# Kernel tuning notes

Measured on AMD Instinct MI355X. Metric: run time of the kernel, lower is better.

Reference implementation:

```python
import jax, jax.numpy as jnp
import numpy as np
from jax import lax

DILATIONS = [1, 2, 4, 8, 16, 32, 64, 128, 256, 512]
L = len(DILATIONS)
T = 2048          # input_size (== sequence length)
C = 128           # residual channels
COND = 16         # condition vector dim
B = 8


def conv1d(x, w, dilation=1):
    # x: [B, T, Cin], w: [K, Cin, Cout] (WIO), SAME padding like keras Conv1D
    return lax.conv_general_dilated(
        x, w, window_strides=(1,), padding='SAME',
        rhs_dilation=(dilation,), dimension_numbers=('NWC', 'WIO', 'NWC'))


def setup_inputs() -> dict:
    key = jax.random.key(0)
    ks = iter(jax.random.split(key, 32))
    n = lambda shape, s=0.05: jax.random.normal(next(ks), shape, dtype=jnp.float32) * s
    inp = {
        'x': jax.random.normal(next(ks), (B, T, 1), dtype=jnp.float32),
        'condition': jax.random.normal(next(ks), (B, COND), dtype=jnp.float32),
        # input projection Conv1D(128, 1)
        'Wc': n((1, 1, C)), 'bc': jnp.zeros((C,), jnp.float32),
        # per-block dilated gated convs Conv1D(128, 3), stacked over L blocks
        'Wt': n((L, 3, C, C)), 'bt': jnp.zeros((L, C), jnp.float32),
        'Ws': n((L, 3, C, C)), 'bs': jnp.zeros((L, C), jnp.float32),
        # stacked conditioning Dense weights: 128 Dense(cond->T) per branch per block
        # Dense i weight [COND, T]; stacked & transposed -> [L, COND, T, 128]
        'Dt': n((L, COND, T, C)), 'Bt': jnp.zeros((L, T, C), jnp.float32),
        'Ds': n((L, COND, T, C)), 'Bs': jnp.zeros((L, T, C), jnp.float32),
        # skip / residual 1x1 convs
        'Wskip': n((L, 1, C, C)), 'bskip': jnp.zeros((L, C), jnp.float32),
        'Wres': n((L, 1, C, C)), 'bres': jnp.zeros((L, C), jnp.float32),
        # output head
        'W1': n((3, C, 2048)), 'b1': jnp.zeros((2048,), jnp.float32),
        'W2': n((3, 2048, 256)), 'b2': jnp.zeros((256,), jnp.float32),
        'W3': n((1, 256, 1)), 'b3': jnp.zeros((1,), jnp.float32),
    }
    return inp


def reference(x, condition, Wc, bc, Wt, bt, Ws, bs, Dt, Bt, Ds, Bs,
              Wskip, bskip, Wres, bres, W1, b1, W2, b2, W3, b3):
    h = conv1d(x, Wc) + bc  # [B, T, 128]
    skip_sum = jnp.zeros_like(h)
    for l, d in enumerate(DILATIONS):
        # fused equivalent of 128 per-channel Dense layers + concat:
        # trans[b,t,k] = condition[b,:] @ Dense_k.W + Dense_k.b
        tt = jnp.einsum('bc,ctk->btk', condition, Dt[l]) + Bt[l]
        ts = jnp.einsum('bc,ctk->btk', condition, Ds[l]) + Bs[l]
        g = jnp.tanh(conv1d(h, Wt[l], d) + bt[l] + tt) * \
            jax.nn.sigmoid(conv1d(h, Ws[l], d) + bs[l] + ts)
        skip_sum = skip_sum + conv1d(g, Wskip[l]) + bskip[l]
        h = conv1d(g, Wres[l]) + bres[l] + h
    out = jax.nn.relu(conv1d(skip_sum, W1) + b1)  # [B, T, 2048]
    out = jax.nn.relu(conv1d(out, W2) + b2)       # [B, T, 256]
    out = jnp.tanh(conv1d(out, W3) + b3)          # [B, T, 1]
    return out
```

## Files before the change

kernel.cpp:

```cpp
#include <hip/hip_runtime.h>
#include <hip/hip_bf16.h>
#include <math.h>

#define T 2048
#define C 128
#define BATCH 8
#define NLAYER 10

typedef short bf16x8 __attribute__((ext_vector_type(8)));
typedef float f32x4 __attribute__((ext_vector_type(4)));
typedef unsigned short u16x4 __attribute__((ext_vector_type(4)));

__device__ __forceinline__ float sigmoidf_(float x) {
    return 1.f / (1.f + __expf(-x));
}
__device__ __forceinline__ float tanhf_(float x) {
    float a = fabsf(x);
    float e = __expf(-2.f * a);
    float t = (1.f - e) / (1.f + e);
    return copysignf(t, x);
}
__device__ __forceinline__ ushort f2bf(float v) {
    __hip_bfloat16 h = __float2bfloat16(v);
    return *reinterpret_cast<ushort*>(&h);
}
__device__ __forceinline__ float bf2f(ushort u) {
    unsigned int x = ((unsigned int)u) << 16;
    return __uint_as_float(x);
}
__device__ __forceinline__ void gl_lds16(const ushort* g, ushort* l) {
    __builtin_amdgcn_global_load_lds(
        (const __attribute__((address_space(1))) unsigned int*)g,
        (__attribute__((address_space(3))) unsigned int*)l, 16, 0, 0);
}

__global__ void k_init(const float* __restrict__ x, const float* __restrict__ Wc,
                       const float* __restrict__ bc, float* __restrict__ h32,
                       ushort* __restrict__ hb, float* __restrict__ skip) {
    int i = blockIdx.x * 256 + threadIdx.x;
    int c = i & 127;
    int pos = i >> 7;
    float v = x[pos] * Wc[c] + bc[c];
    h32[i] = v;
    hb[i] = f2bf(v);
    skip[i] = 0.f;
}

__global__ void k_prep_wgT(const float* __restrict__ Wt, const float* __restrict__ Ws,
                           ushort* __restrict__ WGb) {
    const int tx = threadIdx.x, ty = threadIdx.y;
    const int z = blockIdx.z, s = z & 1, lj = z >> 1;
    const int l = lj / 3, j = lj % 3;
    const float* src = (s ? Ws : Wt) + (size_t)lj * 128 * 128;
    const int col0 = blockIdx.x * 32, ci0 = blockIdx.y * 32;
    __shared__ float tile[32][33];
    #pragma unroll
    for (int i = 0; i < 4; ++i)
        tile[ty + i * 8][tx] = src[(size_t)(ci0 + ty + i * 8) * 128 + col0 + tx];
    __syncthreads();
    #pragma unroll
    for (int i = 0; i < 4; ++i)
        WGb[((size_t)l * 256 + s * 128 + col0 + ty + i * 8) * 384 + j * 128 + ci0 + tx] =
            f2bf(tile[tx][ty + i * 8]);
}
__global__ void k_prep_wrT(const float* __restrict__ Wskip, const float* __restrict__ Wres,
                           ushort* __restrict__ WRb) {
    const int tx = threadIdx.x, ty = threadIdx.y;
    const int z = blockIdx.z, s = z & 1, l = z >> 1;
    const float* src = (s ? Wres : Wskip) + (size_t)l * 128 * 128;
    const int col0 = blockIdx.x * 32, ci0 = blockIdx.y * 32;
    __shared__ float tile[32][33];
    #pragma unroll
    for (int i = 0; i < 4; ++i)
        tile[ty + i * 8][tx] = src[(size_t)(ci0 + ty + i * 8) * 128 + col0 + tx];
    __syncthreads();
    #pragma unroll
    for (int i = 0; i < 4; ++i)
        WRb[((size_t)l * 256 + s * 128 + col0 + ty + i * 8) * 128 + ci0 + tx] =
            f2bf(tile[tx][ty + i * 8]);
}
template<int R>
__global__ void k_prep_wT(const float* __restrict__ W, ushort* __restrict__ Wb, int N) {
    const int tx = threadIdx.x, ty = threadIdx.y;
    const int x = blockIdx.x * 32 + tx;
    const int y0 = blockIdx.y * 32;
    __shared__ float tile[32][33];
    #pragma unroll
    for (int i = 0; i < 4; ++i)
        tile[ty + i * 8][tx] = W[(size_t)(y0 + ty + i * 8) * N + x];
    __syncthreads();
    const int n0 = blockIdx.x * 32;
    #pragma unroll
    for (int i = 0; i < 4; ++i)
        Wb[(size_t)(n0 + ty + i * 8) * R + y0 + tx] = f2bf(tile[tx][ty + i * 8]);
}

__global__ void k_skip_pad(const float* __restrict__ in, ushort* __restrict__ skipp) {
    int i = blockIdx.x * 256 + threadIdx.x;
    int b = i >> 18, rem = i & 262143;
    skipp[(size_t)b * 262400 + 128 + rem] = f2bf(in[i]);
}
__global__ void k_zero_pads(ushort* __restrict__ out1p, ushort* __restrict__ skipp) {
    int i = blockIdx.x * 256 + threadIdx.x;
    if (i < 16384) {
        int ri = i >> 10, col = i & 1023;
        int b = ri >> 1, pr = (ri & 1) ? 2049 : 0;
        ((unsigned int*)out1p)[((size_t)b * 2050 + pr) * 1024 + col] = 0u;
    } else {
        int j = i - 16384;
        int ri = j >> 6, col = j & 63;
        int b = ri >> 1, pr = (ri & 1) ? 2049 : 0;
        ((unsigned int*)skipp)[((size_t)b * 2050 + pr) * 64 + col] = 0u;
    }
}

__global__ __launch_bounds__(256) void k_cond(
    const float* __restrict__ cond,
    const float* __restrict__ Dt, const float* __restrict__ Bt,
    const float* __restrict__ Ds, const float* __restrict__ Bs,
    const float* __restrict__ bt, const float* __restrict__ bs,
    ushort* __restrict__ z0, int l0)
{
    const int br = blockIdx.z;
    const float* D  = br ? Ds : Dt;
    const float* B_ = br ? Bs : Bt;
    const float* b_ = br ? bs : bt;
    const int l  = l0 + blockIdx.y;
    const int ll = blockIdx.y;
    const int k4 = (threadIdx.x & 31) * 4;
    const int tq = threadIdx.x >> 5;
    const int t  = blockIdx.x * 8 + tq;

    __shared__ float sc[128];
    if (threadIdx.x < 128) sc[threadIdx.x] = cond[threadIdx.x];
    __syncthreads();

    const f32x4 bv = *(const f32x4*)(b_ + l * 128 + k4);
    const f32x4 Bv = *(const f32x4*)(B_ + ((size_t)l * T + t) * 128 + k4);

    f32x4 z[8];
    #pragma unroll
    for (int b = 0; b < 8; ++b) z[b] = bv + Bv;

    const float* dp = D + (((size_t)l * 16) * T + t) * 128 + k4;
    #pragma unroll
    for (int c = 0; c < 16; ++c) {
        const f32x4 dv = *(const f32x4*)(dp + (size_t)c * T * 128);
        #pragma unroll
        for (int b = 0; b < 8; ++b)
            z[b] += sc[b * 16 + c] * dv;
    }

    #pragma unroll
    for (int b = 0; b < 8; ++b) {
        size_t zb = (((size_t)ll * 8 + b) * T + t) * 256;
        u16x4 p;
        #pragma unroll
        for (int j = 0; j < 4; ++j) p[j] = f2bf(z[b][j]);
        *(u16x4*)(z0 + zb + br * 128 + k4) = p;
    }
}

__global__ __launch_bounds__(256) void k_gate(
    const float* __restrict__ h32_in, float* __restrict__ h32_out,
    const ushort* __restrict__ hb_in, ushort* __restrict__ hb_out,
    float* __restrict__ skip32,
    const ushort* __restrict__ WG,
    const ushort* __restrict__ WR,
    const ushort* __restrict__ z0l,
    const float* __restrict__ bskip, const float* __restrict__ bres,
    int d)
{
    __shared__ ushort lds[3 * 32 * 136];
    const int tid  = threadIdx.x;
    const int lane = tid & 63, ln16 = lane & 15, quad = lane >> 4;
    const int wave = tid >> 6;
    const int n_off = wave * 64;
    const int t0 = blockIdx.x * 4;

    #pragma unroll
    for (int it = 0; it < 6; ++it) {
        int task = tid + it * 256;
        int part = task & 15;
        int r = (task >> 4) & 31;
        int j = task >> 9;
        int t = t0 + (r >> 3) + (j - 1) * d;
        int b = r & 7;
        uint4 v = make_uint4(0u, 0u, 0u, 0u);
        if (t >= 0 && t < T) v = *(const uint4*)(hb_in + ((size_t)b * T + t) * 128 + part * 8);
        *(uint4*)(&lds[(j * 32 + r) * 136 + part * 8]) = v;
    }
    __syncthreads();

    f32x4 acc[2][4];
    #pragma unroll
    for (int mt = 0; mt < 2; ++mt)
        #pragma unroll
        for (int nt = 0; nt < 4; ++nt)
            acc[mt][nt] = (f32x4){0.f, 0.f, 0.f, 0.f};

    #pragma unroll
    for (int j = 0; j < 3; ++j) {
        #pragma unroll
        for (int kc = 0; kc < 4; ++kc) {
            bf16x8 af[2], bfr[4];
            #pragma unroll
            for (int mt = 0; mt < 2; ++mt)
                af[mt] = *(const bf16x8*)(&lds[(j * 32 + mt * 16 + ln16) * 136 + kc * 32 + quad * 8]);
            #pragma unroll
            for (int nt = 0; nt < 4; ++nt)
                bfr[nt] = *(const bf16x8*)(WG + (size_t)(n_off + nt * 16 + ln16) * 384 + j * 128 + kc * 32 + quad * 8);
            #pragma unroll
            for (int mt = 0; mt < 2; ++mt)
                #pragma unroll
                for (int nt = 0; nt < 4; ++nt)
                    acc[mt][nt] = __builtin_amdgcn_mfma_f32_16x16x32_bf16(af[mt], bfr[nt], acc[mt][nt], 0, 0, 0);
        }
    }
    __syncthreads();

    #pragma unroll
    for (int mt = 0; mt < 2; ++mt) {
        #pragma unroll
        for (int nt = 0; nt < 4; ++nt) {
            int n = n_off + nt * 16 + ln16;
            #pragma unroll
            for (int r4 = 0; r4 < 4; ++r4) {
                int row = mt * 16 + quad * 4 + r4;
                int b = row & 7, p = row >> 3;
                float z = acc[mt][nt][r4] + bf2f(z0l[((size_t)b * T + t0 + p) * 256 + n]);
                lds[row * 264 + n] = f2bf(z);
            }
        }
    }
    __syncthreads();

    {
        int r = tid >> 3;
        int k0 = (tid & 7) * 16;
        #pragma unroll
        for (int kk = 0; kk < 16; ++kk) {
            int k = k0 + kk;
            float zt = bf2f(lds[r * 264 + k]);
            float zs = bf2f(lds[r * 264 + 128 + k]);
            lds[8704 + r * 136 + k] = f2bf(tanhf_(zt) * sigmoidf_(zs));
        }
    }
    __syncthreads();

    f32x4 acc2[2][4];
    #pragma unroll
    for (int mt = 0; mt < 2; ++mt)
        #pragma unroll
        for (int nt = 0; nt < 4; ++nt)
            acc2[mt][nt] = (f32x4){0.f, 0.f, 0.f, 0.f};

    #pragma unroll
    for (int kc = 0; kc < 4; ++kc) {
        bf16x8 af[2], bfr[4];
        #pragma unroll
        for (int mt = 0; mt < 2; ++mt)
            af[mt] = *(const bf16x8*)(&lds[8704 + (mt * 16 + ln16) * 136 + kc * 32 + quad * 8]);
        #pragma unroll
        for (int nt = 0; nt < 4; ++nt)
            bfr[nt] = *(const bf16x8*)(WR + (size_t)(n_off + nt * 16 + ln16) * 128 + kc * 32 + quad * 8);
        #pragma unroll
        for (int mt = 0; mt < 2; ++mt)
            #pragma unroll
            for (int nt = 0; nt < 4; ++nt)
                acc2[mt][nt] = __builtin_amdgcn_mfma_f32_16x16x32_bf16(af[mt], bfr[nt], acc2[mt][nt], 0, 0, 0);
    }

    #pragma unroll
    for (int mt = 0; mt < 2; ++mt) {
        #pragma unroll
        for (int nt = 0; nt < 4; ++nt) {
            int n = n_off + nt * 16 + ln16;
            int k = n & 127;
            #pragma unroll
            for (int r4 = 0; r4 < 4; ++r4) {
                int row = mt * 16 + quad * 4 + r4;
                int b = row & 7, p = row >> 3;
                size_t idx = ((size_t)b * T + t0 + p) * 128 + k;
                float v = acc2[mt][nt][r4];
                if (n < 128) {
                    skip32[idx] += v + bskip[k];
                } else {
                    float hv = v + bres[k] + h32_in[idx];
                    h32_out[idx] = hv;
                    hb_out[idx] = f2bf(hv);
                }
            }
        }
    }
}

#define CV2_AUS 8704
#define CV2_BUF 33280

__global__ __launch_bounds__(256) void k_conv1t(
    const ushort* __restrict__ A,
    const ushort* __restrict__ Wb,
    const float* __restrict__ bias,
    ushort* __restrict__ out1p)
{
    __shared__ ushort sh[2 * CV2_BUF];
    const int tid  = threadIdx.x;
    const int lane = tid & 63, ln16 = lane & 15, quad = lane >> 4;
    const int wave = tid >> 6;
    const int wm = wave >> 1, wn = wave & 1;
    const int m0 = blockIdx.x * 128;
    const int b  = blockIdx.y;
    const int n0 = blockIdx.z * 128;
    const size_t aRow0 = (size_t)b * 2050 + m0;

    f32x4 acc[4][4];
    #pragma unroll
    for (int i = 0; i < 4; ++i)
        #pragma unroll
        for (int j = 0; j < 4; ++j) acc[i][j] = (f32x4){0.f, 0.f, 0.f, 0.f};

    auto stage = [&](int d, int c) {
        const int sb = d * CV2_BUF;
        const int k0 = c * 64;
        #pragma unroll
        for (int ps = 0; ps < 4; ++ps) {
            int task = ps * 256 + tid;
            int r = task >> 3, p = task & 7, q = p ^ (r & 7);
            gl_lds16(A + (aRow0 + r) * 128 + k0 + q * 8,
                     &sh[sb + ((ps * 256 + wave * 64) << 3)]);
        }
        if (tid < 64) {
            int task = 1024 + tid;
            int r = task >> 3, p = task & 7, q = p ^ (r & 7);
            gl_lds16(A + (aRow0 + r) * 128 + k0 + q * 8,
                     &sh[sb + (1024 << 3)]);
        }
        #pragma unroll
        for (int ps = 0; ps < 12; ++ps) {
            int task = ps * 256 + tid;
            int rb = task >> 3, p = task & 7, q = p ^ (rb & 7);
            int nl = rb & 127, tap = rb >> 7;
            gl_lds16(Wb + (size_t)(n0 + nl) * 384 + tap * 128 + k0 + q * 8,
                     &sh[sb + CV2_AUS + ((ps * 256 + wave * 64) << 3)]);
        }
    };

    stage(0, 0);
    __syncthreads();

    for (int c = 0; c < 2; ++c) {
        if (c == 0) stage(1, 1);
        const int sb = (c & 1) * CV2_BUF;
        #pragma unroll
        for (int j = 0; j < 3; ++j) {
            #pragma unroll
            for (int kk = 0; kk < 2; ++kk) {
                bf16x8 af[4], bfr[4];
                #pragma unroll
                for (int mt = 0; mt < 4; ++mt) {
                    int r = wm * 64 + mt * 16 + ln16 + j;
                    int s = (kk << 2) | quad;
                    af[mt] = *(const bf16x8*)(&sh[sb + r * 64 + ((s ^ (r & 7)) << 3)]);
                }
                #pragma unroll
                for (int nt = 0; nt < 4; ++nt) {
                    int rb = j * 128 + wn * 64 + nt * 16 + ln16;
                    int s = (kk << 2) | quad;
                    bfr[nt] = *(const bf16x8*)(&sh[sb + CV2_AUS + rb * 64 + ((s ^ (rb & 7)) << 3)]);
                }
                #pragma unroll
                for (int mt = 0; mt < 4; ++mt)
                    #pragma unroll
                    for (int nt = 0; nt < 4; ++nt)
                        acc[mt][nt] = __builtin_amdgcn_mfma_f32_16x16x32_bf16(af[mt], bfr[nt], acc[mt][nt], 0, 0, 0);
            }
        }
        __syncthreads();
    }

    #pragma unroll
    for (int nt = 0; nt < 4; ++nt) {
        int n = n0 + wn * 64 + nt * 16 + ln16;
        float bv = bias[n];
        #pragma unroll
        for (int mt = 0; mt < 4; ++mt) {
            #pragma unroll
            for (int r4 = 0; r4 < 4; ++r4) {
                int m = wm * 64 + mt * 16 + quad * 4 + r4;
                int t = m0 + m;
                float v = fmaxf(acc[mt][nt][r4] + bv, 0.f);
                out1p[((size_t)b * 2050 + 1 + t) * 2048 + n] = f2bf(v);
            }
        }
    }
}

__global__ __launch_bounds__(256) void k_conv2t(
    const ushort* __restrict__ A,
    const ushort* __restrict__ Wb,
    const float* __restrict__ bias,
    float* __restrict__ out2)
{
    __shared__ ushort sh[2 * CV2_BUF];
    const int tid  = threadIdx.x;
    const int lane = tid & 63, ln16 = lane & 15, quad = lane >> 4;
    const int wave = tid >> 6;
    const int wm = wave >> 1, wn = wave & 1;
    const int m0 = blockIdx.x * 128;
    const int b  = blockIdx.y;
    const int n0 = blockIdx.z * 128;
    const size_t aRow0 = (size_t)b * 2050 + m0;

    f32x4 acc[4][4];
    #pragma unroll
    for (int i = 0; i < 4; ++i)
        #pragma unroll
        for (int j = 0; j < 4; ++j) acc[i][j] = (f32x4){0.f, 0.f, 0.f, 0.f};

    auto stage = [&](int d, int cc) {
        const int sb = d * CV2_BUF;
        const int k0 = cc * 64;
        #pragma unroll
        for (int ps = 0; ps < 4; ++ps) {
            int task = ps * 256 + tid;
            int r = task >> 3, p = task & 7, q = p ^ (r & 7);
            gl_lds16(A + (aRow0 + r) * 2048 + k0 + q * 8,
                     &sh[sb + ((ps * 256 + wave * 64) << 3)]);
        }
        if (tid < 64) {
            int task = 1024 + tid;
            int r = task >> 3, p = task & 7, q = p ^ (r & 7);
            gl_lds16(A + (aRow0 + r) * 2048 + k0 + q * 8,
                     &sh[sb + (1024 << 3)]);
        }
        #pragma unroll
        for (int ps = 0; ps < 12; ++ps) {
            int task = ps * 256 + tid;
            int rb = task >> 3, p = task & 7, q = p ^ (rb & 7);
            int nl = rb & 127, tap = rb >> 7;
            gl_lds16(Wb + (size_t)(n0 + nl) * 6144 + tap * 2048 + k0 + q * 8,
                     &sh[sb + CV2_AUS + ((ps * 256 + wave * 64) << 3)]);
        }
    };

    stage(0, 0);
    __syncthreads();

    for (int cc = 0; cc < 32; ++cc) {
        if (cc < 31) stage((cc + 1) & 1, cc + 1);
        const int sb = (cc & 1) * CV2_BUF;
        #pragma unroll
        for (int j = 0; j < 3; ++j) {
            #pragma unroll
            for (int kk = 0; kk < 2; ++kk) {
                bf16x8 af[4], bfr[4];
                #pragma unroll
                for (int mt = 0; mt < 4; ++mt) {
                    int r = wm * 64 + mt * 16 + ln16 + j;
                    int s = (kk << 2) | quad;
                    af[mt] = *(const bf16x8*)(&sh[sb + r * 64 + ((s ^ (r & 7)) << 3)]);
                }
                #pragma unroll
                for (int nt = 0; nt < 4; ++nt) {
                    int rb = j * 128 + wn * 64 + nt * 16 + ln16;
                    int s = (kk << 2) | quad;
                    bfr[nt] = *(const bf16x8*)(&sh[sb + CV2_AUS + rb * 64 + ((s ^ (rb & 7)) << 3)]);
                }
                #pragma unroll
                for (int mt = 0; mt < 4; ++mt)
                    #pragma unroll
                    for (int nt = 0; nt < 4; ++nt)
                        acc[mt][nt] = __builtin_amdgcn_mfma_f32_16x16x32_bf16(af[mt], bfr[nt], acc[mt][nt], 0, 0, 0);
            }
        }
        __syncthreads();
    }

    #pragma unroll
    for (int nt = 0; nt < 4; ++nt) {
        int n = n0 + wn * 64 + nt * 16 + ln16;
        float bv = bias[n];
        #pragma unroll
        for (int mt = 0; mt < 4; ++mt) {
            #pragma unroll
            for (int r4 = 0; r4 < 4; ++r4) {
                int m = wm * 64 + mt * 16 + quad * 4 + r4;
                int t = m0 + m;
                float v = fmaxf(acc[mt][nt][r4] + bv, 0.f);
                out2[((size_t)b * T + t) * 256 + n] = v;
            }
        }
    }
}

__global__ __launch_bounds__(256) void k_conv3(
    const float* __restrict__ out2, const float* __restrict__ W3,
    const float* __restrict__ b3, float* __restrict__ out)
{
    int wid = threadIdx.x >> 6, lane = threadIdx.x & 63;
    int pos = blockIdx.x * 4 + wid;
    float4 v = *(const float4*)(out2 + (size_t)pos * 256 + lane * 4);
    float4 w = *(const float4*)(W3 + lane * 4);
    float sum = v.x * w.x + v.y * w.y + v.z * w.z + v.w * w.w;
    #pragma unroll
    for (int off = 32; off > 0; off >>= 1) sum += __shfl_down(sum, off);
    if (lane == 0) out[pos] = tanhf_(sum + b3[0]);
}

extern "C" void kernel_launch(void* const* d_in, const int* in_sizes, int n_in,
                              void* d_out, int out_size, void* d_ws, size_t ws_size,
                              hipStream_t stream)
{
    const float* x     = (const float*)d_in[0];
    const float* cond  = (const float*)d_in[1];
    const float* Wc    = (const float*)d_in[2];
    const float* bc    = (const float*)d_in[3];
    const float* Wt    = (const float*)d_in[4];
    const float* bt    = (const float*)d_in[5];
    const float* Ws    = (const float*)d_in[6];
    const float* bs    = (const float*)d_in[7];
    const float* Dt    = (const float*)d_in[8];
    const float* Bt    = (const float*)d_in[9];
    const float* Ds    = (const float*)d_in[10];
    const float* Bs    = (const float*)d_in[11];
    const float* Wskip = (const float*)d_in[12];
    const float* bskip = (const float*)d_in[13];
    const float* Wres  = (const float*)d_in[14];
    const float* bres  = (const float*)d_in[15];
    const float* W1    = (const float*)d_in[16];
    const float* b1    = (const float*)d_in[17];
    const float* W2    = (const float*)d_in[18];
    const float* b2    = (const float*)d_in[19];
    const float* W3    = (const float*)d_in[20];
    const float* b3    = (const float*)d_in[21];
    float* out = (float*)d_out;

    float* ws = (float*)d_ws;
    float*  skip32 = ws;
    float*  h32a   = ws + 2097152;
    float*  h32b   = ws + 4194304;
    float*  out2   = ws + 6291456;
    ushort* u      = (ushort*)(ws + 10485760);
    ushort* hba    = u;
    ushort* hbb    = u + 2097152;
    ushort* WGb    = u + 4194304;
    ushort* WRb    = u + 5177344;
    ushort* W1b    = u + 5505024;
    ushort* W2b    = u + 6291456;
    ushort* skipp  = u;
    ushort* z0     = u + 9961472;
    ushort* out1p  = u + 7864320;

    k_init<<<8192, 256, 0, stream>>>(x, Wc, bc, h32a, hba, skip32);
    k_prep_wgT<<<dim3(4, 4, 60), dim3(32, 8), 0, stream>>>(Wt, Ws, WGb);
    k_prep_wrT<<<dim3(4, 4, 20), dim3(32, 8), 0, stream>>>(Wskip, Wres, WRb);
    k_prep_wT<384><<<dim3(64, 12), dim3(32, 8), 0, stream>>>(W1, W1b, 2048);
    k_prep_wT<6144><<<dim3(8, 192), dim3(32, 8), 0, stream>>>(W2, W2b, 256);

    static const int DIL[NLAYER] = {1, 2, 4, 8, 16, 32, 64, 128, 256, 512};
    float*  h32in = h32a;  float*  h32out = h32b;
    ushort* hbin  = hba;   ushort* hbout  = hbb;

    for (int chunk = 0; chunk < 2; ++chunk) {
        int l0 = chunk * 5;
        k_cond<<<dim3(T / 8, 5, 2), 256, 0, stream>>>(cond, Dt, Bt, Ds, Bs, bt, bs, z0, l0);
        for (int l = l0; l < l0 + 5; ++l) {
            k_gate<<<512, 256, 0, stream>>>(
                h32in, h32out, hbin, hbout, skip32,
                WGb + (size_t)l * 256 * 384,
                WRb + (size_t)l * 256 * 128,
                z0 + (size_t)(l - l0) * 8 * T * 256,
                bskip + l * 128, bres + l * 128,
                DIL[l]);
            float* tf = h32in; h32in = h32out; h32out = tf;
            ushort* tu = hbin; hbin = hbout; hbout = tu;
        }
    }

    k_skip_pad<<<8192, 256, 0, stream>>>(skip32, skipp);
    k_zero_pads<<<68, 256, 0, stream>>>(out1p, skipp);
    k_conv1t<<<dim3(16, 8, 16), 256, 0, stream>>>(skipp, W1b, b1, out1p);
    k_conv2t<<<dim3(16, 8, 2), 256, 0, stream>>>(out1p, W2b, b2, out2);
    k_conv3<<<(BATCH * T) / 4, 256, 0, stream>>>(out2, W3, b3, out);
}
```

Baseline: 868.5 us.

## Defer skip projections into one batched K=1280 GEMM after the residual stack

```diff
diff --git a/kernel.cpp b/kernel.cpp
--- a/kernel.cpp
+++ b/kernel.cpp
@@ -10,6 +10,8 @@
 typedef short bf16x8 __attribute__((ext_vector_type(8)));
 typedef float f32x4 __attribute__((ext_vector_type(4)));
 typedef unsigned short u16x4 __attribute__((ext_vector_type(4)));
+
+struct GPtrs { const ushort* p[NLAYER]; };
 
 __device__ __forceinline__ float sigmoidf_(float x) {
     return 1.f / (1.f + __expf(-x));
@@ -36,14 +38,13 @@
 
 __global__ void k_init(const float* __restrict__ x, const float* __restrict__ Wc,
                        const float* __restrict__ bc, float* __restrict__ h32,
-                       ushort* __restrict__ hb, float* __restrict__ skip) {
+                       ushort* __restrict__ hb) {
     int i = blockIdx.x * 256 + threadIdx.x;
     int c = i & 127;
     int pos = i >> 7;
     float v = x[pos] * Wc[c] + bc[c];
     h32[i] = v;
     hb[i] = f2bf(v);
-    skip[i] = 0.f;
 }
 
 __global__ void k_prep_wgT(const float* __restrict__ Wt, const float* __restrict__ Ws,
@@ -59,12 +60,14 @@
         tile[ty + i * 8][tx] = src[(size_t)(ci0 + ty + i * 8) * 128 + col0 + tx];
     __syncthreads();
     #pragma unroll
-    for (int i = 0; i < 4; ++i)
-        WGb[((size_t)l * 256 + s * 128 + col0 + ty + i * 8) * 384 + j * 128 + ci0 + tx] =
-            f2bf(tile[tx][ty + i * 8]);
-}
-__global__ void k_prep_wrT(const float* __restrict__ Wskip, const float* __restrict__ Wres,
-                           ushort* __restrict__ WRb) {
+    for (int i = 0; i < 4; ++i) {
+        int col = col0 + ty + i * 8;
+        int np = ((col >> 4) * 32) + s * 16 + (col & 15);
+        WGb[((size_t)l * 256 + np) * 384 + j * 128 + ci0 + tx] = f2bf(tile[tx][ty + i * 8]);
+    }
+}
+__global__ void k_prep_wr2(const float* __restrict__ Wskip, const float* __restrict__ Wres,
+                           ushort* __restrict__ WSKb, ushort* __restrict__ WRESb) {
     const int tx = threadIdx.x, ty = threadIdx.y;
     const int z = blockIdx.z, s = z & 1, l = z >> 1;
     const float* src = (s ? Wres : Wskip) + (size_t)l * 128 * 128;
@@ -75,9 +78,12 @@
         tile[ty + i * 8][tx] = src[(size_t)(ci0 + ty + i * 8) * 128 + col0 + tx];
     __syncthreads();
     #pragma unroll
-    for (int i = 0; i < 4; ++i)
-        WRb[((size_t)l * 256 + s * 128 + col0 + ty + i * 8) * 128 + ci0 + tx] =
-            f2bf(tile[tx][ty + i * 8]);
+    for (int i = 0; i < 4; ++i) {
+        int n = col0 + ty + i * 8, ci = ci0 + tx;
+        ushort v = f2bf(tile[tx][ty + i * 8]);
+        if (s) WRESb[((size_t)l * 128 + n) * 128 + ci] = v;
+        else   WSKb[(size_t)n * 1280 + l * 128 + ci] = v;
+    }
 }
 template<int R>
 __global__ void k_prep_wT(const float* __restrict__ W, ushort* __restrict__ Wb, int N) {
@@ -95,11 +101,6 @@
         Wb[(size_t)(n0 + ty + i * 8) * R + y0 + tx] = f2bf(tile[tx][ty + i * 8]);
 }
 
-__global__ void k_skip_pad(const float* __restrict__ in, ushort* __restrict__ skipp) {
-    int i = blockIdx.x * 256 + threadIdx.x;
-    int b = i >> 18, rem = i & 262143;
-    skipp[(size_t)b * 262400 + 128 + rem] = f2bf(in[i]);
-}
 __global__ void k_zero_pads(ushort* __restrict__ out1p, ushort* __restrict__ skipp) {
     int i = blockIdx.x * 256 + threadIdx.x;
     if (i < 16384) {
@@ -151,24 +152,25 @@
             z[b] += sc[b * 16 + c] * dv;
     }
 
+    const int np = ((k4 >> 4) * 32) + br * 16 + (k4 & 15);
     #pragma unroll
     for (int b = 0; b < 8; ++b) {
         size_t zb = (((size_t)ll * 8 + b) * T + t) * 256;
         u16x4 p;
         #pragma unroll
         for (int j = 0; j < 4; ++j) p[j] = f2bf(z[b][j]);
-        *(u16x4*)(z0 + zb + br * 128 + k4) = p;
+        *(u16x4*)(z0 + zb + np) = p;
     }
 }
 
 __global__ __launch_bounds__(256) void k_gate(
     const float* __restrict__ h32_in, float* __restrict__ h32_out,
     const ushort* __restrict__ hb_in, ushort* __restrict__ hb_out,
-    float* __restrict__ skip32,
     const ushort* __restrict__ WG,
-    const ushort* __restrict__ WR,
+    const ushort* __restrict__ WRES,
     const ushort* __restrict__ z0l,
-    const float* __restrict__ bskip, const float* __restrict__ bres,
+    ushort* __restrict__ gout,
+    const float* __restrict__ bres,
     int d)
 {
     __shared__ ushort lds[3 * 32 * 136];
@@ -190,6 +192,23 @@
         if (t >= 0 && t < T) v = *(const uint4*)(hb_in + ((size_t)b * T + t) * 128 + part * 8);
         *(uint4*)(&lds[(j * 32 + r) * 136 + part * 8]) = v;
     }
+
+    ushort zre[2][4][4];
+    float hpre[2][2][4];
+    #pragma unroll
+    for (int mt = 0; mt < 2; ++mt) {
+        #pragma unroll
+        for (int r4 = 0; r4 < 4; ++r4) {
+            int row = mt * 16 + quad * 4 + r4;
+            int b = row & 7, p = row >> 3;
+            const ushort* zp = z0l + ((size_t)b * T + t0 + p) * 256 + n_off + ln16;
+            #pragma unroll
+            for (int nt = 0; nt < 4; ++nt) zre[mt][nt][r4] = zp[nt * 16];
+            const float* hp = h32_in + ((size_t)b * T + t0 + p) * 128 + wave * 32 + ln16;
+            #pragma unroll
+            for (int n2 = 0; n2 < 2; ++n2) hpre[mt][n2][r4] = hp[n2 * 16];
+        }
+    }
     __syncthreads();
 
     f32x4 acc[2][4];
@@ -217,79 +236,162 @@
                     acc[mt][nt] = __builtin_amdgcn_mfma_f32_16x16x32_bf16(af[mt], bfr[nt], acc[mt][nt], 0, 0, 0);
         }
     }
-    __syncthreads();
-
-    #pragma unroll
-    for (int mt = 0; mt < 2; ++mt) {
-        #pragma unroll
-        for (int nt = 0; nt < 4; ++nt) {
-            int n = n_off + nt * 16 + ln16;
+
+    ushort gfr[2][2][4];
+    #pragma unroll
+    for (int mt = 0; mt < 2; ++mt)
+        #pragma unroll
+        for (int i = 0; i < 2; ++i)
+            #pragma unroll
+            for (int r4 = 0; r4 < 4; ++r4) {
+                float zt = acc[mt][2 * i][r4]     + bf2f(zre[mt][2 * i][r4]);
+                float zs = acc[mt][2 * i + 1][r4] + bf2f(zre[mt][2 * i + 1][r4]);
+                gfr[mt][i][r4] = f2bf(tanhf_(zt) * sigmoidf_(zs));
+            }
+    #pragma unroll
+    for (int mt = 0; mt < 2; ++mt)
+        #pragma unroll
+        for (int i = 0; i < 2; ++i)
             #pragma unroll
             for (int r4 = 0; r4 < 4; ++r4) {
                 int row = mt * 16 + quad * 4 + r4;
                 int b = row & 7, p = row >> 3;
-                float z = acc[mt][nt][r4] + bf2f(z0l[((size_t)b * T + t0 + p) * 256 + n]);
-                lds[row * 264 + n] = f2bf(z);
-            }
-        }
-    }
-    __syncthreads();
-
-    {
-        int r = tid >> 3;
-        int k0 = (tid & 7) * 16;
-        #pragma unroll
-        for (int kk = 0; kk < 16; ++kk) {
-            int k = k0 + kk;
-            float zt = bf2f(lds[r * 264 + k]);
-            float zs = bf2f(lds[r * 264 + 128 + k]);
-            lds[8704 + r * 136 + k] = f2bf(tanhf_(zt) * sigmoidf_(zs));
-        }
-    }
-    __syncthreads();
-
-    f32x4 acc2[2][4];
+                gout[((size_t)b * T + t0 + p) * 128 + wave * 32 + i * 16 + ln16] = gfr[mt][i][r4];
+            }
+    __syncthreads();
+
     #pragma unroll
     for (int mt = 0; mt < 2; ++mt)
         #pragma unroll
-        for (int nt = 0; nt < 4; ++nt)
-            acc2[mt][nt] = (f32x4){0.f, 0.f, 0.f, 0.f};
+        for (int i = 0; i < 2; ++i)
+            #pragma unroll
+            for (int r4 = 0; r4 < 4; ++r4) {
+                int row = mt * 16 + quad * 4 + r4;
+                lds[8704 + row * 136 + wave * 32 + i * 16 + ln16] = gfr[mt][i][r4];
+            }
+    __syncthreads();
+
+    f32x4 acc2[2][2];
+    #pragma unroll
+    for (int mt = 0; mt < 2; ++mt)
+        #pragma unroll
+        for (int n2 = 0; n2 < 2; ++n2)
+            acc2[mt][n2] = (f32x4){0.f, 0.f, 0.f, 0.f};
 
     #pragma unroll
     for (int kc = 0; kc < 4; ++kc) {
-        bf16x8 af[2], bfr[4];
+        bf16x8 af[2], bfr[2];
         #pragma unroll
         for (int mt = 0; mt < 2; ++mt)
             af[mt] = *(const bf16x8*)(&lds[8704 + (mt * 16 + ln16) * 136 + kc * 32 + quad * 8]);
         #pragma unroll
-        for (int nt = 0; nt < 4; ++nt)
-            bfr[nt] = *(const bf16x8*)(WR + (size_t)(n_off + nt * 16 + ln16) * 128 + kc * 32 + quad * 8);
+        for (int n2 = 0; n2 < 2; ++n2)
+            bfr[n2] = *(const bf16x8*)(WRES + (size_t)(wave * 32 + n2 * 16 + ln16) * 128 + kc * 32 + quad * 8);
         #pragma unroll
         for (int mt = 0; mt < 2; ++mt)
             #pragma unroll
-            for (int nt = 0; nt < 4; ++nt)
-                acc2[mt][nt] = __builtin_amdgcn_mfma_f32_16x16x32_bf16(af[mt], bfr[nt], acc2[mt][nt], 0, 0, 0);
-    }
-
-    #pragma unroll
-    for (int mt = 0; mt < 2; ++mt) {
-        #pragma unroll
-        for (int nt = 0; nt < 4; ++nt) {
-            int n = n_off + nt * 16 + ln16;
-            int k = n & 127;
+            for (int n2 = 0; n2 < 2; ++n2)
+                acc2[mt][n2] = __builtin_amdgcn_mfma_f32_16x16x32_bf16(af[mt], bfr[n2], acc2[mt][n2], 0, 0, 0);
+    }
+
+    #pragma unroll
+    for (int n2 = 0; n2 < 2; ++n2) {
+        int n = wave * 32 + n2 * 16 + ln16;
+        float bv = bres[n];
+        #pragma unroll
+        for (int mt = 0; mt < 2; ++mt) {
             #pragma unroll
             for (int r4 = 0; r4 < 4; ++r4) {
                 int row = mt * 16 + quad * 4 + r4;
                 int b = row & 7, p = row >> 3;
-                size_t idx = ((size_t)b * T + t0 + p) * 128 + k;
-                float v = acc2[mt][nt][r4];
-                if (n < 128) {
-                    skip32[idx] += v + bskip[k];
-                } else {
-                    float hv = v + bres[k] + h32_in[idx];
-                    h32_out[idx] = hv;
-                    hb_out[idx] = f2bf(hv);
-                }
+                size_t idx = ((size_t)b * T + t0 + p) * 128 + n;
+                float hv = acc2[mt][n2][r4] + bv + hpre[mt][n2][r4];
+                h32_out[idx] = hv;
+                hb_out[idx] = f2bf(hv);
+            }
+        }
+    }
+}
+
+__global__ __launch_bounds__(256) void k_skipsum(
+    GPtrs gp, const ushort* __restrict__ Wsk,
+    const float* __restrict__ bskip,
+    ushort* __restrict__ skipp)
+{
+    __shared__ ushort sh[2 * 12288];
+    const int tid  = threadIdx.x;
+    const int lane = tid & 63, ln16 = lane & 15, quad = lane >> 4;
+    const int wave = tid >> 6;
+    const int wm = wave >> 1, wn = wave & 1;
+    const int m0 = blockIdx.x * 64;
+    const int b  = blockIdx.y;
+
+    f32x4 acc[2][4];
+    #pragma unroll
+    for (int i = 0; i < 2; ++i)
+        #pragma unroll
+        for (int j = 0; j < 4; ++j) acc[i][j] = (f32x4){0.f, 0.f, 0.f, 0.f};
+
+    auto stage = [&](int dd, int kc) {
+        const int sb = dd * 12288;
+        const int l = kc >> 1, k0 = (kc & 1) * 64;
+        const ushort* gl = gp.p[l] + ((size_t)b * T + m0) * 128 + k0;
+        #pragma unroll
+        for (int ps = 0; ps < 2; ++ps) {
+            int task = ps * 256 + tid;
+            int r = task >> 3, p = task & 7, q = p ^ (r & 7);
+            gl_lds16(gl + (size_t)r * 128 + q * 8, &sh[sb + ((ps * 256 + wave * 64) << 3)]);
+        }
+        #pragma unroll
+        for (int ps = 0; ps < 4; ++ps) {
+            int task = ps * 256 + tid;
+            int r = task >> 3, p = task & 7, q = p ^ (r & 7);
+            gl_lds16(Wsk + (size_t)r * 1280 + l * 128 + k0 + q * 8,
+                     &sh[sb + 4096 + ((ps * 256 + wave * 64) << 3)]);
+        }
+    };
+
+    stage(0, 0);
+    __syncthreads();
+
+    for (int kc = 0; kc < 20; ++kc) {
+        if (kc < 19) stage((kc + 1) & 1, kc + 1);
+        const int sb = (kc & 1) * 12288;
+        #pragma unroll
+        for (int kk = 0; kk < 2; ++kk) {
+            bf16x8 af[2], bfr[4];
+            int s = (kk << 2) | quad;
+            #pragma unroll
+            for (int mt = 0; mt < 2; ++mt) {
+                int r = wm * 32 + mt * 16 + ln16;
+                af[mt] = *(const bf16x8*)(&sh[sb + r * 64 + ((s ^ (r & 7)) << 3)]);
+            }
+            #pragma unroll
+            for (int nt = 0; nt < 4; ++nt) {
+                int rb = wn * 64 + nt * 16 + ln16;
+                bfr[nt] = *(const bf16x8*)(&sh[sb + 4096 + rb * 64 + ((s ^ (rb & 7)) << 3)]);
+            }
+            #pragma unroll
+            for (int mt = 0; mt < 2; ++mt)
+                #pragma unroll
+                for (int nt = 0; nt < 4; ++nt)
+                    acc[mt][nt] = __builtin_amdgcn_mfma_f32_16x16x32_bf16(af[mt], bfr[nt], acc[mt][nt], 0, 0, 0);
+        }
+        __syncthreads();
+    }
+
+    #pragma unroll
+    for (int nt = 0; nt < 4; ++nt) {
+        int n = wn * 64 + nt * 16 + ln16;
+        float bv = 0.f;
+        #pragma unroll
+        for (int l = 0; l < NLAYER; ++l) bv += bskip[l * 128 + n];
+        #pragma unroll
+        for (int mt = 0; mt < 2; ++mt) {
+            #pragma unroll
+            for (int r4 = 0; r4 < 4; ++r4) {
+                int t = m0 + wm * 32 + mt * 16 + quad * 4 + r4;
+                skipp[((size_t)b * 2050 + 1 + t) * 128 + n] = f2bf(acc[mt][nt][r4] + bv);
             }
         }
     }
@@ -320,8 +422,8 @@
         #pragma unroll
         for (int j = 0; j < 4; ++j) acc[i][j] = (f32x4){0.f, 0.f, 0.f, 0.f};
 
-    auto stage = [&](int d, int c) {
-        const int sb = d * CV2_BUF;
+    auto stage = [&](int dd, int c) {
+        const int sb = dd * CV2_BUF;
         const int k0 = c * 64;
         #pragma unroll
         for (int ps = 0; ps < 4; ++ps) {
@@ -418,8 +520,8 @@
         #pragma unroll
         for (int j = 0; j < 4; ++j) acc[i][j] = (f32x4){0.f, 0.f, 0.f, 0.f};
 
-    auto stage = [&](int d, int cc) {
-        const int sb = d * CV2_BUF;
+    auto stage = [&](int dd, int cc) {
+        const int sb = dd * CV2_BUF;
         const int k0 = cc * 64;
         #pragma unroll
         for (int ps = 0; ps < 4; ++ps) {
@@ -536,25 +638,31 @@
     const float* b3    = (const float*)d_in[21];
     float* out = (float*)d_out;
 
-    float* ws = (float*)d_ws;
-    float*  skip32 = ws;
-    float*  h32a   = ws + 2097152;
-    float*  h32b   = ws + 4194304;
-    float*  out2   = ws + 6291456;
-    ushort* u      = (ushort*)(ws + 10485760);
-    ushort* hba    = u;
-    ushort* hbb    = u + 2097152;
-    ushort* WGb    = u + 4194304;
-    ushort* WRb    = u + 5177344;
-    ushort* W1b    = u + 5505024;
-    ushort* W2b    = u + 6291456;
-    ushort* skipp  = u;
-    ushort* z0     = u + 9961472;
-    ushort* out1p  = u + 7864320;
-
-    k_init<<<8192, 256, 0, stream>>>(x, Wc, bc, h32a, hba, skip32);
+    char* wsb = (char*)d_ws;
+    float*  h32a  = (float*)(wsb + 0);
+    float*  h32b  = (float*)(wsb + 8388608);
+    float*  out2  = (float*)(wsb + 16777216);
+    ushort* hba   = (ushort*)(wsb + 33554432);
+    ushort* hbb   = (ushort*)(wsb + 37748736);
+    ushort* WGb   = (ushort*)(wsb + 41943040);
+    ushort* WRESb = (ushort*)(wsb + 43909120);
+    ushort* W1b   = (ushort*)(wsb + 44236800);
+    ushort* W2b   = (ushort*)(wsb + 45809664);
+    ushort* WSKb  = (ushort*)(wsb + 48955392);
+    ushort* z0    = (ushort*)(wsb + 49283072);
+    GPtrs gp;
+    ushort* gw[NLAYER];
+    for (int l = 0; l < 4; ++l)
+        gw[l] = (ushort*)(wsb + 16777216 + (size_t)l * 4194304);
+    for (int l = 4; l < NLAYER; ++l)
+        gw[l] = (ushort*)(wsb + 91226112 + (size_t)(l - 4) * 4194304);
+    for (int l = 0; l < NLAYER; ++l) gp.p[l] = gw[l];
+    ushort* skipp = hba;
+    ushort* out1p = z0;
+
+    k_init<<<8192, 256, 0, stream>>>(x, Wc, bc, h32a, hba);
     k_prep_wgT<<<dim3(4, 4, 60), dim3(32, 8), 0, stream>>>(Wt, Ws, WGb);
-    k_prep_wrT<<<dim3(4, 4, 20), dim3(32, 8), 0, stream>>>(Wskip, Wres, WRb);
+    k_prep_wr2<<<dim3(4, 4, 20), dim3(32, 8), 0, stream>>>(Wskip, Wres, WSKb, WRESb);
     k_prep_wT<384><<<dim3(64, 12), dim3(32, 8), 0, stream>>>(W1, W1b, 2048);
     k_prep_wT<6144><<<dim3(8, 192), dim3(32, 8), 0, stream>>>(W2, W2b, 256);
 
@@ -567,18 +675,19 @@
         k_cond<<<dim3(T / 8, 5, 2), 256, 0, stream>>>(cond, Dt, Bt, Ds, Bs, bt, bs, z0, l0);
         for (int l = l0; l < l0 + 5; ++l) {
             k_gate<<<512, 256, 0, stream>>>(
-                h32in, h32out, hbin, hbout, skip32,
+                h32in, h32out, hbin, hbout,
                 WGb + (size_t)l * 256 * 384,
-                WRb + (size_t)l * 256 * 128,
+                WRESb + (size_t)l * 128 * 128,
                 z0 + (size_t)(l - l0) * 8 * T * 256,
-                bskip + l * 128, bres + l * 128,
+                gw[l],
+                bres + l * 128,
                 DIL[l]);
             float* tf = h32in; h32in = h32out; h32out = tf;
             ushort* tu = hbin; hbin = hbout; hbout = tu;
         }
     }
 
-    k_skip_pad<<<8192, 256, 0, stream>>>(skip32, skipp);
+    k_skipsum<<<dim3(32, 8), 256, 0, stream>>>(gp, WSKb, bskip, skipp);
     k_zero_pads<<<68, 256, 0, stream>>>(out1p, skipp);
     k_conv1t<<<dim3(16, 8, 16), 256, 0, stream>>>(skipp, W1b, b1, out1p);
     k_conv2t<<<dim3(16, 8, 2), 256, 0, stream>>>(out1p, W2b, b2, out2);
```

Result: faster. 812.2 us (-6.5%).
